# Performance work log

Hardware: AMD Instinct MI355X
Metric: run time of the kernel (lower is better)

## Reference

```python
import jax, jax.numpy as jnp
import numpy as np

# Dimensions (match init_kwargs / input_specs)
B, T, D, H, HH, E, L = 256, 512, 256, 256, 128, 32, 2


def setup_inputs() -> dict:
    key = jax.random.key(0)
    ks = jax.random.split(key, 8)
    f32 = jnp.float32
    s_ih = 1.0 / np.sqrt(D)
    s_hh = 1.0 / np.sqrt(H)
    s_hy = 1.0 / np.sqrt(D + H)
    s_hh_hy = 1.0 / np.sqrt(HH)
    s_z = 1.0 / np.sqrt(HH)
    s_d = 1.0 / np.sqrt(E)
    return {
        "input": jax.random.normal(ks[0], (B, T, D), f32),
        # main-cell weights, stacked over layers (layer1 input = hidden = D)
        "Wih": jax.random.normal(ks[1], (L, H, D), f32) * s_ih,
        "Whh": jax.random.normal(ks[2], (L, H, H), f32) * s_hh,
        "b": jnp.zeros((L, H), f32),
        # hyper (meta) RNN cell: input is concat(x_t, h_{t-1})
        "Wih_hy": jax.random.normal(ks[3], (L, HH, D + H), f32) * s_hy,
        "Whh_hy": jax.random.normal(ks[4], (L, HH, HH), f32) * s_hh_hy,
        "b_hy": jnp.zeros((L, HH), f32),
        # embedding projections: hyper_h -> z for (x-scale, h-scale, bias), then z -> d
        "Whz": jax.random.normal(ks[5], (L, 3, E, HH), f32) * s_z,
        "bz": jnp.ones((L, 3, E), f32),  # init z to 1 so d starts near a plain RNN
        "Wzd": jax.random.normal(ks[6], (L, 3, H, E), f32) * s_d,
    }


def reference(input, Wih, Whh, b, Wih_hy, Whh_hy, b_hy, Whz, bz, Wzd):
    """MetaRNN (HyperNetwork-conditioned RNN): for each layer, a small hyper RNN
    consumes [x_t, h_{t-1}] and emits embeddings z that generate per-unit scales
    d_x, d_h and a dynamic bias d_b for the main tanh RNN cell.
    Returns (all hidden states [B,T,H], last hidden state [B,H])."""
    Bb = input.shape[0]
    dt = input.dtype
    x_seq = input
    for l in range(L):
        # input-to-hidden GEMM for the whole sequence, hoisted out of the scan
        xW = jnp.einsum('btd,hd->bth', x_seq, Wih[l])  # [B,T,H]
        Whh_l, b_l = Whh[l], b[l]
        Wih_hy_l, Whh_hy_l, b_hy_l = Wih_hy[l], Whh_hy[l], b_hy[l]
        Whz_l, bz_l, Wzd_l = Whz[l], bz[l], Wzd[l]

        def step(carry, inp):
            h, hh = carry           # main hidden [B,H], hyper hidden [B,HH]
            x_t, xW_t = inp
            hyp_in = jnp.concatenate([x_t, h], axis=1)          # [B, D+H]
            hh_new = jnp.tanh(hyp_in @ Wih_hy_l.T + hh @ Whh_hy_l.T + b_hy_l)
            z = jnp.einsum('bk,gek->bge', hh_new, Whz_l) + bz_l  # [B,3,E]
            d = jnp.einsum('bge,ghe->bgh', z, Wzd_l)             # [B,3,H]
            h_new = jnp.tanh(d[:, 0] * xW_t + d[:, 1] * (h @ Whh_l.T)
                             + d[:, 2] + b_l)
            return (h_new, hh_new), h_new

        h0 = jnp.zeros((Bb, H), dt)
        hh0 = jnp.zeros((Bb, HH), dt)
        xs = (jnp.swapaxes(x_seq, 0, 1), jnp.swapaxes(xW, 0, 1))  # time-major
        _, ys = jax.lax.scan(step, (h0, hh0), xs)
        x_seq = jnp.swapaxes(ys, 0, 1)  # [B,T,H]
    return (x_seq, x_seq[:, -1, :])
```

## Files before the change

kernel.cpp:

```cpp
#include <hip/hip_runtime.h>


#define DEVI __device__ __forceinline__

typedef __bf16 bf16x8 __attribute__((ext_vector_type(8)));
typedef float f32x4 __attribute__((ext_vector_type(4)));
typedef unsigned short u16;
typedef unsigned int u32;
typedef u32 u32x4 __attribute__((ext_vector_type(4)));
typedef u16 u16x8 __attribute__((ext_vector_type(8)));

constexpr int B_ = 256, T_ = 512, D_ = 256, H_ = 256, HH_ = 128, E_ = 32;
constexpr int BT = B_ * T_;

constexpr int OXW = 0,      PXW = 16 * 8 * 512;
constexpr int OXH = 131072, PXH = 8 * 8 * 512;
constexpr int OHY = 196608, PHY = 8 * 12 * 512;
constexpr int OWHH = 294912, PWHH = 16 * 8 * 512;
constexpr int OWHZ = 425984, PWHZ = 6 * 4 * 512;
constexpr int OWZD = 450560, PWZD = 48 * 512;
constexpr int LSTRIDE = 499712;

constexpr size_t WS_XW = 0;
constexpr size_t WS_XH = (size_t)BT * H_ * 4;
constexpr size_t WS_FR = WS_XH + (size_t)BT * HH_ * 4;

DEVI u16 f2bf(float v) {
  u32 u = __float_as_uint(v);
  u += 0x7fffu + ((u >> 16) & 1u);
  return (u16)(u >> 16);
}
DEVI float bf2f(u16 s) { return __uint_as_float(((u32)s) << 16); }
DEVI void split2(float v, u16 &hi, u16 &lo) {
  hi = f2bf(v);
  lo = f2bf(v - bf2f(hi));
}
DEVI bf16x8 ldfrag(const u16 *p) {
  u32x4 v = *reinterpret_cast<const u32x4 *>(p);
  return __builtin_bit_cast(bf16x8, v);
}
DEVI void pin(bf16x8 &x) {
  u32x4 t = __builtin_bit_cast(u32x4, x);
  asm volatile("" : "+v"(t));
  x = __builtin_bit_cast(bf16x8, t);
}
DEVI f32x4 mfma3(bf16x8 ah, bf16x8 al, bf16x8 bh, bf16x8 bl, f32x4 c) {
  c = __builtin_amdgcn_mfma_f32_16x16x32_bf16(ah, bh, c, 0, 0, 0);
  c = __builtin_amdgcn_mfma_f32_16x16x32_bf16(ah, bl, c, 0, 0, 0);
  c = __builtin_amdgcn_mfma_f32_16x16x32_bf16(al, bh, c, 0, 0, 0);
  return c;
}
DEVI float tanh_fast(float x) {
  float e = __expf(2.0f * x);
  return 1.0f - 2.0f / (e + 1.0f);
}
DEVI void block_sync() {
  asm volatile("s_waitcnt lgkmcnt(0)\n\ts_barrier" ::: "memory");
}

__global__ void metarnn_prep(const float *__restrict__ Wih,
                             const float *__restrict__ Whh,
                             const float *__restrict__ Wih_hy,
                             const float *__restrict__ Whh_hy,
                             const float *__restrict__ Whz,
                             const float *__restrict__ Wzd,
                             u16 *__restrict__ fr) {
  int gid = blockIdx.x * 256 + threadIdx.x;
  int lane = gid & 63;
  int e = gid >> 6;
  if (e >= 2 * 488) return;
  int l = e / 488, r = e - l * 488;
  u16 *base = fr + (size_t)l * LSTRIDE;
  int rowL = lane & 15, kg = (lane >> 4) << 3;

  const float *src = nullptr;
  int ld = 0, nt = 0, kt = 0, KT = 1, special = 0;
  u16 *dh = nullptr, *dl = nullptr;
  if (r < 128) {
    nt = r >> 3; kt = r & 7; KT = 8;
    src = Wih + (size_t)l * H_ * D_; ld = D_;
    dh = base + OXW; dl = dh + PXW;
  } else if (r < 192) {
    r -= 128; nt = r >> 3; kt = r & 7; KT = 8;
    src = Wih_hy + (size_t)l * HH_ * (D_ + H_); ld = D_ + H_;
    dh = base + OXH; dl = dh + PXH;
  } else if (r < 288) {
    r -= 192; nt = r / 12; kt = r - nt * 12; KT = 12; special = 1;
    dh = base + OHY; dl = dh + PHY;
  } else if (r < 416) {
    r -= 288; nt = r >> 3; kt = r & 7; KT = 8;
    src = Whh + (size_t)l * H_ * H_; ld = H_;
    dh = base + OWHH; dl = dh + PWHH;
  } else if (r < 440) {
    r -= 416; nt = r >> 2; kt = r & 3; KT = 4;
    src = Whz + (size_t)l * 3 * E_ * HH_; ld = HH_;
    dh = base + OWHZ; dl = dh + PWHZ;
  } else {
    r -= 440; int g = r >> 4; nt = r & 15; kt = 0; KT = 1;
    src = Wzd + (size_t)(l * 3 + g) * H_ * E_; ld = E_;
    dh = base + OWZD + g * 16 * 512; dl = base + OWZD + PWZD + g * 16 * 512;
  }
  int row = nt * 16 + rowL;
  long dof = ((long)(nt * KT + kt) * 64 + lane) * 8;
  for (int j = 0; j < 8; ++j) {
    int k = kt * 32 + kg + j;
    float v;
    if (special) {
      v = (k < 256) ? Wih_hy[((size_t)l * HH_ + row) * (D_ + H_) + 256 + k]
                    : Whh_hy[((size_t)l * HH_ + row) * HH_ + (k - 256)];
    } else {
      v = src[(size_t)row * ld + k];
    }
    u16 hi, lo;
    split2(v, hi, lo);
    dh[dof + j] = hi;
    dl[dof + j] = lo;
  }
}

__global__ __launch_bounds__(256, 1) void metarnn_gemm(
    const float *__restrict__ x, const u16 *__restrict__ fr,
    float *__restrict__ xW, float *__restrict__ xH) {
  int w = threadIdx.x >> 6, lane = threadIdx.x & 63;
  int m0 = blockIdx.x * 32;
  int rowL = lane & 15, kg = (lane >> 4) << 3;
  f32x4 acc[2][6] = {};
  const u16 *fxw_h = fr + OXW, *fxw_l = fxw_h + PXW;
  const u16 *fxh_h = fr + OXH, *fxh_l = fxh_h + PXH;

  for (int kt = 0; kt < 8; ++kt) {
    bf16x8 ah[2], al[2];
    for (int s = 0; s < 2; ++s) {
      const float *xp = x + (size_t)(m0 + s * 16 + rowL) * 256 + kt * 32 + kg;
      u16x8 vh, vl;
#pragma unroll
      for (int j = 0; j < 8; ++j) {
        u16 hi, lo;
        split2(xp[j], hi, lo);
        vh[j] = hi; vl[j] = lo;
      }
      ah[s] = __builtin_bit_cast(bf16x8, vh);
      al[s] = __builtin_bit_cast(bf16x8, vl);
    }
#pragma unroll
    for (int q = 0; q < 6; ++q) {
      int nt = w * 6 + q;
      long o = (nt < 16) ? ((long)(nt * 8 + kt) * 64 + lane) * 8
                         : ((long)((nt - 16) * 8 + kt) * 64 + lane) * 8;
      const u16 *bh = (nt < 16) ? fxw_h + o : fxh_h + o;
      const u16 *bl = (nt < 16) ? fxw_l + o : fxh_l + o;
      bf16x8 B0 = ldfrag(bh), B1 = ldfrag(bl);
      acc[0][q] = mfma3(ah[0], al[0], B0, B1, acc[0][q]);
      acc[1][q] = mfma3(ah[1], al[1], B0, B1, acc[1][q]);
    }
  }
  for (int s = 0; s < 2; ++s)
    for (int q = 0; q < 6; ++q) {
      int nt = w * 6 + q;
#pragma unroll
      for (int r = 0; r < 4; ++r) {
        int row = m0 + s * 16 + (lane >> 4) * 4 + r;
        if (nt < 16)
          xW[(size_t)row * H_ + nt * 16 + rowL] = acc[s][q][r];
        else
          xH[(size_t)row * HH_ + (nt - 16) * 16 + rowL] = acc[s][q][r];
      }
    }
}

__global__ __launch_bounds__(512, 2) void metarnn_scan(
    const float *__restrict__ xW, const float *__restrict__ xH,
    const u16 *__restrict__ fr, const float *__restrict__ bmain,
    const float *__restrict__ bhy, const float *__restrict__ bz,
    float *__restrict__ y, float *__restrict__ hlast, int layer, int isLast) {
  __shared__ __align__(16) u16 hc_h[8 * 512];
  __shared__ __align__(16) u16 hc_l[8 * 512];
  __shared__ __align__(16) u16 hhb_h[2][4 * 512];
  __shared__ __align__(16) u16 hhb_l[2][4 * 512];
  __shared__ __align__(16) u16 zf_h[3 * 512];
  __shared__ __align__(16) u16 zf_l[3 * 512];
  __shared__ __align__(16) u16 hy_lds[8 * 12 * 512];

  int tid = threadIdx.x, w = tid >> 6, lane = tid & 63;
  int bs = blockIdx.x * 16;
  int rowL = lane & 15, colG = lane >> 4;

  const u16 *FHY = fr + OHY, *FHYl = FHY + PHY;
  const u16 *FWH = fr + OWHH, *FWHl = FWH + PWHH;
  const u16 *FWZ = fr + OWHZ, *FWZl = FWZ + PWHZ;
  const u16 *FZD = fr + OWZD, *FZDl = FZD + PWZD;

  for (int i = tid; i < 8 * 512; i += 512) { hc_h[i] = 0; hc_l[i] = 0; }
  for (int i = tid; i < 4 * 512; i += 512) {
    hhb_h[0][i] = 0; hhb_l[0][i] = 0; hhb_h[1][i] = 0; hhb_l[1][i] = 0;
  }
  for (int i = tid; i < 3 * 512; i += 512) { zf_h[i] = 0; zf_l[i] = 0; }
  for (int i = tid; i < 8 * 12 * 512 / 8; i += 512) {
    *reinterpret_cast<u32x4 *>(&hy_lds[(size_t)i * 8]) =
        *reinterpret_cast<const u32x4 *>(FHY + (size_t)i * 8);
  }

  bf16x8 RWH[2][8], RWL[2][8];
#pragma unroll
  for (int p = 0; p < 2; ++p)
#pragma unroll
    for (int kt = 0; kt < 8; ++kt) {
      long o = ((long)((2 * w + p) * 8 + kt) * 64 + lane) * 8;
      RWH[p][kt] = ldfrag(FWH + o);  pin(RWH[p][kt]);
      RWL[p][kt] = ldfrag(FWHl + o); pin(RWL[p][kt]);
    }
  bf16x8 zresH[4], zresL[4];
  {
    int wz = (w < 6) ? w : 0;
#pragma unroll
    for (int kk = 0; kk < 4; ++kk) {
      long o = ((long)(wz * 4 + kk) * 64 + lane) * 8;
      zresH[kk] = ldfrag(FWZ + o);  pin(zresH[kk]);
      zresL[kk] = ldfrag(FWZl + o); pin(zresL[kk]);
    }
  }

  int c2 = 16 * w + rowL;
  float bhv = bhy[layer * HH_ + c2];
  float bzv = (w < 6) ? bz[layer * 3 * E_ + c2] : 0.0f;
  float bbv[2];
  bbv[0] = bmain[layer * H_ + 32 * w + rowL];
  bbv[1] = bmain[layer * H_ + 32 * w + 16 + rowL];

  bf16x8 bYL[4];
#define LOAD_Y(PTR, S, KT)                                                    \
  bYL[S] = ldfrag((PTR) + ((long)(w * 12 + (KT)) * 64 + lane) * 8);
#pragma unroll
  for (int s = 0; s < 4; ++s) { LOAD_Y(FHYl, s, s) }

  float xhv[4], xwv[2][4];
#pragma unroll
  for (int r = 0; r < 4; ++r) {
    size_t row = (size_t)(bs + 4 * colG + r) * T_;
    xhv[r] = xH[row * HH_ + c2];
    xwv[0][r] = xW[row * H_ + 32 * w + rowL];
    xwv[1][r] = xW[row * H_ + 32 * w + 16 + rowL];
  }

  __syncthreads();

  for (int t = 0; t < T_; ++t) {
    const int pr = t & 1;
    const u16 *fhyl = FHYl, *fzd = FZD, *fzdl = FZDl;
    asm volatile("" : "+s"(fhyl), "+s"(fzd), "+s"(fzdl));

    f32x4 aAe = {}, aAo = {}, aW0 = {}, aW1 = {};
    __builtin_amdgcn_s_setprio(1);
#pragma unroll
    for (int j = 0; j < 12; ++j) {
      const int s4 = j & 3;
      bf16x8 ah, al;
      if (j < 8) {
        ah = ldfrag(&hc_h[j * 512 + lane * 8]);
        al = ldfrag(&hc_l[j * 512 + lane * 8]);
      } else {
        ah = ldfrag(&hhb_h[pr ^ 1][(j - 8) * 512 + lane * 8]);
        al = ldfrag(&hhb_l[pr ^ 1][(j - 8) * 512 + lane * 8]);
      }
      bf16x8 yh = ldfrag(&hy_lds[(w * 12 + j) * 512 + lane * 8]);
      if (j & 1) aAo = mfma3(ah, al, yh, bYL[s4], aAo);
      else       aAe = mfma3(ah, al, yh, bYL[s4], aAe);
      if (j < 8) {
        aW0 = mfma3(ah, al, RWH[0][j], RWL[0][j], aW0);
        aW1 = mfma3(ah, al, RWH[1][j], RWL[1][j], aW1);
        LOAD_Y(fhyl, s4, j + 4)
      } else {
        LOAD_Y(fhyl, s4, j - 8)
      }
    }
    __builtin_amdgcn_s_setprio(0);
    f32x4 aA;
#pragma unroll
    for (int r = 0; r < 4; ++r) aA[r] = aAe[r] + aAo[r];

    bf16x8 D0h[2], D0l[2];
#pragma unroll
    for (int p = 0; p < 2; ++p) {
      long o = ((long)(2 * w + p) * 64 + lane) * 8;
      D0h[p] = ldfrag(fzd + o);
      D0l[p] = ldfrag(fzdl + o);
    }

    {
      int kfr = w >> 1;
      int hb2 = 2 * (w & 1) + (rowL >> 3);
      int j7 = rowL & 7;
#pragma unroll
      for (int r = 0; r < 4; ++r) {
        float v = tanh_fast(aA[r] + xhv[r] + bhv);
        u16 hi, lo;
        split2(v, hi, lo);
        int di = kfr * 512 + ((4 * colG + r) + 16 * hb2) * 8 + j7;
        hhb_h[pr][di] = hi;
        hhb_l[pr][di] = lo;
      }
    }
#pragma unroll
    for (int r = 0; r < 4; ++r) {
      xhv[r] = xH[((size_t)(bs + 4 * colG + r) * T_ + t + 1) * HH_ + c2];
    }
    block_sync();

    bf16x8 D1h[2], D1l[2], D2h[2], D2l[2];
#pragma unroll
    for (int p = 0; p < 2; ++p) {
      long o1 = ((long)(16 + 2 * w + p) * 64 + lane) * 8;
      long o2 = ((long)(32 + 2 * w + p) * 64 + lane) * 8;
      D1h[p] = ldfrag(fzd + o1);
      D1l[p] = ldfrag(fzdl + o1);
      D2h[p] = ldfrag(fzd + o2);
      D2l[p] = ldfrag(fzdl + o2);
    }

    if (w < 6) {
      f32x4 aZ = {};
#pragma unroll
      for (int kk = 0; kk < 4; ++kk) {
        bf16x8 ah = ldfrag(&hhb_h[pr][kk * 512 + lane * 8]);
        bf16x8 al = ldfrag(&hhb_l[pr][kk * 512 + lane * 8]);
        aZ = mfma3(ah, al, zresH[kk], zresL[kk], aZ);
      }
      int g = c2 >> 5;
      int hb3 = 2 * (w & 1) + (rowL >> 3);
      int j7 = rowL & 7;
#pragma unroll
      for (int r = 0; r < 4; ++r) {
        float v = aZ[r] + bzv;
        u16 hi, lo;
        split2(v, hi, lo);
        int di = g * 512 + ((4 * colG + r) + 16 * hb3) * 8 + j7;
        zf_h[di] = hi;
        zf_l[di] = lo;
      }
    }
    block_sync();

    float arg[2][4];
#pragma unroll
    for (int p = 0; p < 2; ++p)
#pragma unroll
      for (int r = 0; r < 4; ++r) arg[p][r] = bbv[p];
    {
      bf16x8 zh = ldfrag(&zf_h[0 * 512 + lane * 8]);
      bf16x8 zl = ldfrag(&zf_l[0 * 512 + lane * 8]);
#pragma unroll
      for (int p = 0; p < 2; ++p) {
        f32x4 zero = {};
        f32x4 dg = mfma3(zh, zl, D0h[p], D0l[p], zero);
#pragma unroll
        for (int r = 0; r < 4; ++r) arg[p][r] += dg[r] * xwv[p][r];
      }
    }
#pragma unroll
    for (int r = 0; r < 4; ++r) {
      size_t row = (size_t)(bs + 4 * colG + r) * T_ + t + 1;
      xwv[0][r] = xW[row * H_ + 32 * w + rowL];
      xwv[1][r] = xW[row * H_ + 32 * w + 16 + rowL];
    }
    {
      bf16x8 zh = ldfrag(&zf_h[1 * 512 + lane * 8]);
      bf16x8 zl = ldfrag(&zf_l[1 * 512 + lane * 8]);
#pragma unroll
      for (int p = 0; p < 2; ++p) {
        f32x4 zero = {};
        f32x4 dg = mfma3(zh, zl, D1h[p], D1l[p], zero);
#pragma unroll
        for (int r = 0; r < 4; ++r)
          arg[p][r] += dg[r] * ((p == 0) ? aW0[r] : aW1[r]);
      }
    }
    {
      bf16x8 zh = ldfrag(&zf_h[2 * 512 + lane * 8]);
      bf16x8 zl = ldfrag(&zf_l[2 * 512 + lane * 8]);
#pragma unroll
      for (int p = 0; p < 2; ++p) {
        f32x4 zero = {};
        f32x4 dg = mfma3(zh, zl, D2h[p], D2l[p], zero);
#pragma unroll
        for (int r = 0; r < 4; ++r) arg[p][r] += dg[r];
      }
    }

#pragma unroll
    for (int p = 0; p < 2; ++p) {
      int c = 32 * w + 16 * p + rowL;
      int hb6 = 2 * p + (rowL >> 3);
      int j7 = rowL & 7;
#pragma unroll
      for (int r = 0; r < 4; ++r) {
        int m = 4 * colG + r;
        float h = tanh_fast(arg[p][r]);
        size_t gi = (size_t)(bs + m) * T_ + t;
        y[gi * H_ + c] = h;
        if (isLast && t == T_ - 1) hlast[(size_t)(bs + m) * H_ + c] = h;
        u16 hi, lo;
        split2(h, hi, lo);
        int di = (c >> 5) * 512 + (m + 16 * hb6) * 8 + j7;
        hc_h[di] = hi;
        hc_l[di] = lo;
      }
    }
    block_sync();
  }
#undef LOAD_Y
}

extern "C" void kernel_launch(void *const *d_in, const int *in_sizes, int n_in,
                              void *d_out, int out_size, void *d_ws,
                              size_t ws_size, hipStream_t stream) {
  (void)in_sizes; (void)n_in; (void)out_size; (void)ws_size;
  const float *input  = (const float *)d_in[0];
  const float *Wih    = (const float *)d_in[1];
  const float *Whh    = (const float *)d_in[2];
  const float *b      = (const float *)d_in[3];
  const float *Wih_hy = (const float *)d_in[4];
  const float *Whh_hy = (const float *)d_in[5];
  const float *b_hy   = (const float *)d_in[6];
  const float *Whz    = (const float *)d_in[7];
  const float *bz     = (const float *)d_in[8];
  const float *Wzd    = (const float *)d_in[9];

  float *out = (float *)d_out;
  float *xW = (float *)((char *)d_ws + WS_XW);
  float *xH = (float *)((char *)d_ws + WS_XH);
  u16 *fr = (u16 *)((char *)d_ws + WS_FR);
  float *hlast = out + (size_t)BT * H_;

  metarnn_prep<<<dim3(244), dim3(256), 0, stream>>>(Wih, Whh, Wih_hy, Whh_hy,
                                                    Whz, Wzd, fr);
  for (int l = 0; l < 2; ++l) {
    const float *xsrc = (l == 0) ? input : out;
    const u16 *frl = fr + (size_t)l * LSTRIDE;
    metarnn_gemm<<<dim3(BT / 32), dim3(256), 0, stream>>>(xsrc, frl, xW, xH);
    metarnn_scan<<<dim3(16), dim3(512), 0, stream>>>(
        xW, xH, frl, b, b_hy, bz, out, hlast, l, (l == 1) ? 1 : 0);
  }
}
```

Baseline: 9.273 ms.

## Split scan block into hyper and main warp groups with streamed weights

The scan kernel now runs 16 waves per block instead of 8. Waves 0-7 compute the hyper-RNN recurrence and waves 8-15 compute the main h@Whh product, so the two serial GEMM chains run concurrently. Weights are no longer staged in LDS or pinned in registers. Each wave instead streams its fragments from global memory through a small rotating register buffer, which lowers register pressure but adds global/L2 load latency inside the per-timestep loop.

```diff
diff --git a/kernel.cpp b/kernel.cpp
--- a/kernel.cpp
+++ b/kernel.cpp
@@ -38,11 +38,6 @@
 DEVI bf16x8 ldfrag(const u16 *p) {
   u32x4 v = *reinterpret_cast<const u32x4 *>(p);
   return __builtin_bit_cast(bf16x8, v);
-}
-DEVI void pin(bf16x8 &x) {
-  u32x4 t = __builtin_bit_cast(u32x4, x);
-  asm volatile("" : "+v"(t));
-  x = __builtin_bit_cast(bf16x8, t);
 }
 DEVI f32x4 mfma3(bf16x8 ah, bf16x8 al, bf16x8 bh, bf16x8 bl, f32x4 c) {
   c = __builtin_amdgcn_mfma_f32_16x16x32_bf16(ah, bh, c, 0, 0, 0);
@@ -168,162 +163,150 @@
     }
 }
 
-__global__ __launch_bounds__(512, 2) void metarnn_scan(
+__global__ __launch_bounds__(1024, 4) void metarnn_scan(
     const float *__restrict__ xW, const float *__restrict__ xH,
     const u16 *__restrict__ fr, const float *__restrict__ bmain,
     const float *__restrict__ bhy, const float *__restrict__ bz,
     float *__restrict__ y, float *__restrict__ hlast, int layer, int isLast) {
-  __shared__ __align__(16) u16 hc_h[8 * 512];
-  __shared__ __align__(16) u16 hc_l[8 * 512];
-  __shared__ __align__(16) u16 hhb_h[2][4 * 512];
-  __shared__ __align__(16) u16 hhb_l[2][4 * 512];
-  __shared__ __align__(16) u16 zf_h[3 * 512];
-  __shared__ __align__(16) u16 zf_l[3 * 512];
-  __shared__ __align__(16) u16 hy_lds[8 * 12 * 512];
+  __shared__ __align__(16) u16 hc_h[8 * 512], hc_l[8 * 512];
+  __shared__ __align__(16) u16 hhb_h[2][4 * 512], hhb_l[2][4 * 512];
+  __shared__ __align__(16) u16 zf_h[3 * 512], zf_l[3 * 512];
 
   int tid = threadIdx.x, w = tid >> 6, lane = tid & 63;
   int bs = blockIdx.x * 16;
   int rowL = lane & 15, colG = lane >> 4;
+  const bool hyper = (w < 8);
+  const int mi = w & 7;
 
   const u16 *FHY = fr + OHY, *FHYl = FHY + PHY;
   const u16 *FWH = fr + OWHH, *FWHl = FWH + PWHH;
   const u16 *FWZ = fr + OWHZ, *FWZl = FWZ + PWHZ;
   const u16 *FZD = fr + OWZD, *FZDl = FZD + PWZD;
 
-  for (int i = tid; i < 8 * 512; i += 512) { hc_h[i] = 0; hc_l[i] = 0; }
-  for (int i = tid; i < 4 * 512; i += 512) {
+  for (int i = tid; i < 8 * 512; i += 1024) { hc_h[i] = 0; hc_l[i] = 0; }
+  for (int i = tid; i < 4 * 512; i += 1024) {
     hhb_h[0][i] = 0; hhb_l[0][i] = 0; hhb_h[1][i] = 0; hhb_l[1][i] = 0;
   }
-  for (int i = tid; i < 3 * 512; i += 512) { zf_h[i] = 0; zf_l[i] = 0; }
-  for (int i = tid; i < 8 * 12 * 512 / 8; i += 512) {
-    *reinterpret_cast<u32x4 *>(&hy_lds[(size_t)i * 8]) =
-        *reinterpret_cast<const u32x4 *>(FHY + (size_t)i * 8);
-  }
-
-  bf16x8 RWH[2][8], RWL[2][8];
-#pragma unroll
-  for (int p = 0; p < 2; ++p)
-#pragma unroll
-    for (int kt = 0; kt < 8; ++kt) {
-      long o = ((long)((2 * w + p) * 8 + kt) * 64 + lane) * 8;
-      RWH[p][kt] = ldfrag(FWH + o);  pin(RWH[p][kt]);
-      RWL[p][kt] = ldfrag(FWHl + o); pin(RWL[p][kt]);
-    }
-  bf16x8 zresH[4], zresL[4];
-  {
-    int wz = (w < 6) ? w : 0;
-#pragma unroll
-    for (int kk = 0; kk < 4; ++kk) {
-      long o = ((long)(wz * 4 + kk) * 64 + lane) * 8;
-      zresH[kk] = ldfrag(FWZ + o);  pin(zresH[kk]);
-      zresL[kk] = ldfrag(FWZl + o); pin(zresL[kk]);
-    }
-  }
-
-  int c2 = 16 * w + rowL;
-  float bhv = bhy[layer * HH_ + c2];
+  for (int i = tid; i < 3 * 512; i += 1024) { zf_h[i] = 0; zf_l[i] = 0; }
+
+  int c2 = 16 * (w & 7) + rowL;
+  float bhv = hyper ? bhy[layer * HH_ + c2] : 0.0f;
   float bzv = (w < 6) ? bz[layer * 3 * E_ + c2] : 0.0f;
-  float bbv[2];
-  bbv[0] = bmain[layer * H_ + 32 * w + rowL];
-  bbv[1] = bmain[layer * H_ + 32 * w + 16 + rowL];
-
-  bf16x8 bYL[4];
-#define LOAD_Y(PTR, S, KT)                                                    \
-  bYL[S] = ldfrag((PTR) + ((long)(w * 12 + (KT)) * 64 + lane) * 8);
-#pragma unroll
-  for (int s = 0; s < 4; ++s) { LOAD_Y(FHYl, s, s) }
-
-  float xhv[4], xwv[2][4];
-#pragma unroll
-  for (int r = 0; r < 4; ++r) {
-    size_t row = (size_t)(bs + 4 * colG + r) * T_;
-    xhv[r] = xH[row * HH_ + c2];
-    xwv[0][r] = xW[row * H_ + 32 * w + rowL];
-    xwv[1][r] = xW[row * H_ + 32 * w + 16 + rowL];
+  float bbv0 = 0.0f, bbv1 = 0.0f;
+  if (!hyper) {
+    bbv0 = bmain[layer * H_ + 32 * mi + rowL];
+    bbv1 = bmain[layer * H_ + 32 * mi + 16 + rowL];
+  }
+
+  bf16x8 S[12];
+  bf16x8 Z[8];
+  if (hyper) {
+#pragma unroll
+    for (int s = 0; s < 3; ++s) {
+      long o = ((long)(w * 12 + s) * 64 + lane) * 8;
+      S[s] = ldfrag(FHY + o);
+      S[3 + s] = ldfrag(FHYl + o);
+    }
+  } else {
+#pragma unroll
+    for (int s = 0; s < 3; ++s)
+#pragma unroll
+      for (int p = 0; p < 2; ++p) {
+        long o = ((long)((2 * mi + p) * 8 + s) * 64 + lane) * 8;
+        S[4 * s + p] = ldfrag(FWH + o);
+        S[4 * s + 2 + p] = ldfrag(FWHl + o);
+      }
+  }
+
+  float xv[8];
+  if (hyper) {
+#pragma unroll
+    for (int r = 0; r < 4; ++r)
+      xv[r] = xH[((size_t)(bs + 4 * colG + r) * T_) * HH_ + c2];
+  } else {
+#pragma unroll
+    for (int r = 0; r < 4; ++r) {
+      size_t row = (size_t)(bs + 4 * colG + r) * T_;
+      xv[r] = xW[row * H_ + 32 * mi + rowL];
+      xv[4 + r] = xW[row * H_ + 32 * mi + 16 + rowL];
+    }
   }
 
   __syncthreads();
 
   for (int t = 0; t < T_; ++t) {
     const int pr = t & 1;
-    const u16 *fhyl = FHYl, *fzd = FZD, *fzdl = FZDl;
-    asm volatile("" : "+s"(fhyl), "+s"(fzd), "+s"(fzdl));
-
-    f32x4 aAe = {}, aAo = {}, aW0 = {}, aW1 = {};
-    __builtin_amdgcn_s_setprio(1);
-#pragma unroll
-    for (int j = 0; j < 12; ++j) {
-      const int s4 = j & 3;
-      bf16x8 ah, al;
-      if (j < 8) {
-        ah = ldfrag(&hc_h[j * 512 + lane * 8]);
-        al = ldfrag(&hc_l[j * 512 + lane * 8]);
-      } else {
-        ah = ldfrag(&hhb_h[pr ^ 1][(j - 8) * 512 + lane * 8]);
-        al = ldfrag(&hhb_l[pr ^ 1][(j - 8) * 512 + lane * 8]);
-      }
-      bf16x8 yh = ldfrag(&hy_lds[(w * 12 + j) * 512 + lane * 8]);
-      if (j & 1) aAo = mfma3(ah, al, yh, bYL[s4], aAo);
-      else       aAe = mfma3(ah, al, yh, bYL[s4], aAe);
-      if (j < 8) {
-        aW0 = mfma3(ah, al, RWH[0][j], RWL[0][j], aW0);
-        aW1 = mfma3(ah, al, RWH[1][j], RWL[1][j], aW1);
-        LOAD_Y(fhyl, s4, j + 4)
-      } else {
-        LOAD_Y(fhyl, s4, j - 8)
-      }
-    }
-    __builtin_amdgcn_s_setprio(0);
-    f32x4 aA;
-#pragma unroll
-    for (int r = 0; r < 4; ++r) aA[r] = aAe[r] + aAo[r];
-
-    bf16x8 D0h[2], D0l[2];
-#pragma unroll
-    for (int p = 0; p < 2; ++p) {
-      long o = ((long)(2 * w + p) * 64 + lane) * 8;
-      D0h[p] = ldfrag(fzd + o);
-      D0l[p] = ldfrag(fzdl + o);
-    }
-
-    {
-      int kfr = w >> 1;
-      int hb2 = 2 * (w & 1) + (rowL >> 3);
-      int j7 = rowL & 7;
-#pragma unroll
-      for (int r = 0; r < 4; ++r) {
-        float v = tanh_fast(aA[r] + xhv[r] + bhv);
-        u16 hi, lo;
-        split2(v, hi, lo);
-        int di = kfr * 512 + ((4 * colG + r) + 16 * hb2) * 8 + j7;
-        hhb_h[pr][di] = hi;
-        hhb_l[pr][di] = lo;
-      }
-    }
-#pragma unroll
-    for (int r = 0; r < 4; ++r) {
-      xhv[r] = xH[((size_t)(bs + 4 * colG + r) * T_ + t + 1) * HH_ + c2];
+    f32x4 acc0 = {}, acc1 = {};
+
+    if (hyper) {
+      __builtin_amdgcn_s_setprio(1);
+#pragma unroll
+      for (int j = 0; j < 12; ++j) {
+        const int s = j % 3;
+        bf16x8 ah, al;
+        if (j < 8) {
+          ah = ldfrag(&hc_h[j * 512 + lane * 8]);
+          al = ldfrag(&hc_l[j * 512 + lane * 8]);
+        } else {
+          ah = ldfrag(&hhb_h[pr ^ 1][(j - 8) * 512 + lane * 8]);
+          al = ldfrag(&hhb_l[pr ^ 1][(j - 8) * 512 + lane * 8]);
+        }
+        if (j & 1) acc1 = mfma3(ah, al, S[s], S[3 + s], acc1);
+        else       acc0 = mfma3(ah, al, S[s], S[3 + s], acc0);
+        const int ktp = (j < 9) ? j + 3 : j - 9;
+        long o = ((long)(w * 12 + ktp) * 64 + lane) * 8;
+        S[s] = ldfrag(FHY + o);
+        S[3 + s] = ldfrag(FHYl + o);
+      }
+      __builtin_amdgcn_s_setprio(0);
+      {
+        int kfr = w >> 1;
+        int hb2 = 2 * (w & 1) + (rowL >> 3);
+        int j7 = rowL & 7;
+#pragma unroll
+        for (int r = 0; r < 4; ++r) {
+          float v = tanh_fast((acc0[r] + acc1[r]) + xv[r] + bhv);
+          u16 hi, lo;
+          split2(v, hi, lo);
+          int di = kfr * 512 + ((4 * colG + r) + 16 * hb2) * 8 + j7;
+          hhb_h[pr][di] = hi;
+          hhb_l[pr][di] = lo;
+        }
+      }
+    } else {
+      __builtin_amdgcn_s_setprio(1);
+#pragma unroll
+      for (int j = 0; j < 8; ++j) {
+        const int s = j % 3;
+        bf16x8 ah = ldfrag(&hc_h[j * 512 + lane * 8]);
+        bf16x8 al = ldfrag(&hc_l[j * 512 + lane * 8]);
+        acc0 = mfma3(ah, al, S[4 * s + 0], S[4 * s + 2], acc0);
+        acc1 = mfma3(ah, al, S[4 * s + 1], S[4 * s + 3], acc1);
+        const int ktp = (j < 5) ? j + 3 : ((j == 5) ? 2 : ((j == 6) ? 0 : 1));
+#pragma unroll
+        for (int p = 0; p < 2; ++p) {
+          long o = ((long)((2 * mi + p) * 8 + ktp) * 64 + lane) * 8;
+          S[4 * s + p] = ldfrag(FWH + o);
+          S[4 * s + 2 + p] = ldfrag(FWHl + o);
+        }
+      }
+      __builtin_amdgcn_s_setprio(0);
     }
     block_sync();
 
-    bf16x8 D1h[2], D1l[2], D2h[2], D2l[2];
-#pragma unroll
-    for (int p = 0; p < 2; ++p) {
-      long o1 = ((long)(16 + 2 * w + p) * 64 + lane) * 8;
-      long o2 = ((long)(32 + 2 * w + p) * 64 + lane) * 8;
-      D1h[p] = ldfrag(fzd + o1);
-      D1l[p] = ldfrag(fzdl + o1);
-      D2h[p] = ldfrag(fzd + o2);
-      D2l[p] = ldfrag(fzdl + o2);
-    }
-
     if (w < 6) {
+#pragma unroll
+      for (int kk = 0; kk < 4; ++kk) {
+        long o = ((long)(w * 4 + kk) * 64 + lane) * 8;
+        Z[kk] = ldfrag(FWZ + o);
+        Z[4 + kk] = ldfrag(FWZl + o);
+      }
       f32x4 aZ = {};
 #pragma unroll
       for (int kk = 0; kk < 4; ++kk) {
         bf16x8 ah = ldfrag(&hhb_h[pr][kk * 512 + lane * 8]);
         bf16x8 al = ldfrag(&hhb_l[pr][kk * 512 + lane * 8]);
-        aZ = mfma3(ah, al, zresH[kk], zresL[kk], aZ);
+        aZ = mfma3(ah, al, Z[kk], Z[4 + kk], aZ);
       }
       int g = c2 >> 5;
       int hb3 = 2 * (w & 1) + (rowL >> 3);
@@ -338,76 +321,108 @@
         zf_l[di] = lo;
       }
     }
+    if (!hyper) {
+#pragma unroll
+      for (int p = 0; p < 2; ++p) {
+        long o = ((long)(2 * mi + p) * 64 + lane) * 8;
+        Z[p] = ldfrag(FZD + o);
+        Z[2 + p] = ldfrag(FZDl + o);
+      }
+    }
     block_sync();
 
-    float arg[2][4];
-#pragma unroll
-    for (int p = 0; p < 2; ++p)
-#pragma unroll
-      for (int r = 0; r < 4; ++r) arg[p][r] = bbv[p];
-    {
-      bf16x8 zh = ldfrag(&zf_h[0 * 512 + lane * 8]);
-      bf16x8 zl = ldfrag(&zf_l[0 * 512 + lane * 8]);
+    if (hyper) {
+      const int tn = (t + 1 < T_) ? t + 1 : t;
+#pragma unroll
+      for (int r = 0; r < 4; ++r)
+        xv[r] = xH[((size_t)(bs + 4 * colG + r) * T_ + tn) * HH_ + c2];
+    } else {
+      float arg[2][4];
+#pragma unroll
+      for (int r = 0; r < 4; ++r) { arg[0][r] = bbv0; arg[1][r] = bbv1; }
+      {
+        bf16x8 zh = ldfrag(&zf_h[lane * 8]);
+        bf16x8 zl = ldfrag(&zf_l[lane * 8]);
+        f32x4 dg0[2];
+#pragma unroll
+        for (int p = 0; p < 2; ++p) {
+          f32x4 zero = {};
+          dg0[p] = mfma3(zh, zl, Z[p], Z[2 + p], zero);
+        }
+#pragma unroll
+        for (int p = 0; p < 2; ++p) {
+          long o = ((long)(16 + 2 * mi + p) * 64 + lane) * 8;
+          Z[4 + p] = ldfrag(FZD + o);
+          Z[6 + p] = ldfrag(FZDl + o);
+        }
+#pragma unroll
+        for (int p = 0; p < 2; ++p)
+#pragma unroll
+          for (int r = 0; r < 4; ++r) arg[p][r] += dg0[p][r] * xv[p * 4 + r];
+      }
+      {
+        bf16x8 zh = ldfrag(&zf_h[512 + lane * 8]);
+        bf16x8 zl = ldfrag(&zf_l[512 + lane * 8]);
+        f32x4 dg1[2];
+#pragma unroll
+        for (int p = 0; p < 2; ++p) {
+          f32x4 zero = {};
+          dg1[p] = mfma3(zh, zl, Z[4 + p], Z[6 + p], zero);
+        }
+#pragma unroll
+        for (int p = 0; p < 2; ++p) {
+          long o = ((long)(32 + 2 * mi + p) * 64 + lane) * 8;
+          Z[p] = ldfrag(FZD + o);
+          Z[2 + p] = ldfrag(FZDl + o);
+        }
+#pragma unroll
+        for (int r = 0; r < 4; ++r) {
+          arg[0][r] += dg1[0][r] * acc0[r];
+          arg[1][r] += dg1[1][r] * acc1[r];
+        }
+      }
+      {
+        bf16x8 zh = ldfrag(&zf_h[2 * 512 + lane * 8]);
+        bf16x8 zl = ldfrag(&zf_l[2 * 512 + lane * 8]);
+#pragma unroll
+        for (int p = 0; p < 2; ++p) {
+          f32x4 zero = {};
+          f32x4 dg = mfma3(zh, zl, Z[p], Z[2 + p], zero);
+#pragma unroll
+          for (int r = 0; r < 4; ++r) arg[p][r] += dg[r];
+        }
+      }
+      {
+        const int tn = (t + 1 < T_) ? t + 1 : t;
+#pragma unroll
+        for (int r = 0; r < 4; ++r) {
+          size_t row = (size_t)(bs + 4 * colG + r) * T_ + tn;
+          xv[r] = xW[row * H_ + 32 * mi + rowL];
+          xv[4 + r] = xW[row * H_ + 32 * mi + 16 + rowL];
+        }
+      }
 #pragma unroll
       for (int p = 0; p < 2; ++p) {
-        f32x4 zero = {};
-        f32x4 dg = mfma3(zh, zl, D0h[p], D0l[p], zero);
-#pragma unroll
-        for (int r = 0; r < 4; ++r) arg[p][r] += dg[r] * xwv[p][r];
-      }
-    }
-#pragma unroll
-    for (int r = 0; r < 4; ++r) {
-      size_t row = (size_t)(bs + 4 * colG + r) * T_ + t + 1;
-      xwv[0][r] = xW[row * H_ + 32 * w + rowL];
-      xwv[1][r] = xW[row * H_ + 32 * w + 16 + rowL];
-    }
-    {
-      bf16x8 zh = ldfrag(&zf_h[1 * 512 + lane * 8]);
-      bf16x8 zl = ldfrag(&zf_l[1 * 512 + lane * 8]);
-#pragma unroll
-      for (int p = 0; p < 2; ++p) {
-        f32x4 zero = {};
-        f32x4 dg = mfma3(zh, zl, D1h[p], D1l[p], zero);
-#pragma unroll
-        for (int r = 0; r < 4; ++r)
-          arg[p][r] += dg[r] * ((p == 0) ? aW0[r] : aW1[r]);
-      }
-    }
-    {
-      bf16x8 zh = ldfrag(&zf_h[2 * 512 + lane * 8]);
-      bf16x8 zl = ldfrag(&zf_l[2 * 512 + lane * 8]);
-#pragma unroll
-      for (int p = 0; p < 2; ++p) {
-        f32x4 zero = {};
-        f32x4 dg = mfma3(zh, zl, D2h[p], D2l[p], zero);
-#pragma unroll
-        for (int r = 0; r < 4; ++r) arg[p][r] += dg[r];
-      }
-    }
-
-#pragma unroll
-    for (int p = 0; p < 2; ++p) {
-      int c = 32 * w + 16 * p + rowL;
-      int hb6 = 2 * p + (rowL >> 3);
-      int j7 = rowL & 7;
-#pragma unroll
-      for (int r = 0; r < 4; ++r) {
-        int m = 4 * colG + r;
-        float h = tanh_fast(arg[p][r]);
-        size_t gi = (size_t)(bs + m) * T_ + t;
-        y[gi * H_ + c] = h;
-        if (isLast && t == T_ - 1) hlast[(size_t)(bs + m) * H_ + c] = h;
-        u16 hi, lo;
-        split2(h, hi, lo);
-        int di = (c >> 5) * 512 + (m + 16 * hb6) * 8 + j7;
-        hc_h[di] = hi;
-        hc_l[di] = lo;
+        int c = 32 * mi + 16 * p + rowL;
+        int hb6 = 2 * p + (rowL >> 3);
+        int j7 = rowL & 7;
+#pragma unroll
+        for (int r = 0; r < 4; ++r) {
+          int m = 4 * colG + r;
+          float h = tanh_fast(arg[p][r]);
+          size_t gi = (size_t)(bs + m) * T_ + t;
+          y[gi * H_ + c] = h;
+          if (isLast && t == T_ - 1) hlast[(size_t)(bs + m) * H_ + c] = h;
+          u16 hi, lo;
+          split2(h, hi, lo);
+          int di = (c >> 5) * 512 + (m + 16 * hb6) * 8 + j7;
+          hc_h[di] = hi;
+          hc_l[di] = lo;
+        }
       }
     }
     block_sync();
   }
-#undef LOAD_Y
 }
 
 extern "C" void kernel_launch(void *const *d_in, const int *in_sizes, int n_in,
@@ -437,7 +452,7 @@
     const float *xsrc = (l == 0) ? input : out;
     const u16 *frl = fr + (size_t)l * LSTRIDE;
     metarnn_gemm<<<dim3(BT / 32), dim3(256), 0, stream>>>(xsrc, frl, xW, xH);
-    metarnn_scan<<<dim3(16), dim3(512), 0, stream>>>(
+    metarnn_scan<<<dim3(16), dim3(1024), 0, stream>>>(
         xW, xH, frl, b, b_hy, bz, out, hlast, l, (l == 1) ? 1 : 0);
   }
 }
```

Measured after the change: 17.39 ms. +87.5%, slower.

## Stream Whh-hi and Whz fragments from global instead of pinning in registers

Applied to the files above, without the earlier changes.

Stops keeping the high half of the recurrent weight fragments and the z-projection fragments resident in registers. Instead it streams them from global/L2 through a rotating 3-slot buffer inside the main loop, and deepens the hyper-weight prefetch ring from 4 to 6 slots. Per-timestep xH/xW loads are now double-buffered and issued earlier, and the loads that guarded out-of-range t+1 reads are clamped. This relieves register pressure on the serial recurrence, at the cost of extra per-step global traffic and load latency on the critical path.

```diff
diff --git a/kernel.cpp b/kernel.cpp
--- a/kernel.cpp
+++ b/kernel.cpp
@@ -200,60 +200,58 @@
         *reinterpret_cast<const u32x4 *>(FHY + (size_t)i * 8);
   }
 
-  bf16x8 RWH[2][8], RWL[2][8];
+  bf16x8 RWL[2][8];
 #pragma unroll
   for (int p = 0; p < 2; ++p)
 #pragma unroll
     for (int kt = 0; kt < 8; ++kt) {
       long o = ((long)((2 * w + p) * 8 + kt) * 64 + lane) * 8;
-      RWH[p][kt] = ldfrag(FWH + o);  pin(RWH[p][kt]);
-      RWL[p][kt] = ldfrag(FWHl + o); pin(RWL[p][kt]);
-    }
-  bf16x8 zresH[4], zresL[4];
-  {
-    int wz = (w < 6) ? w : 0;
-#pragma unroll
-    for (int kk = 0; kk < 4; ++kk) {
-      long o = ((long)(wz * 4 + kk) * 64 + lane) * 8;
-      zresH[kk] = ldfrag(FWZ + o);  pin(zresH[kk]);
-      zresL[kk] = ldfrag(FWZl + o); pin(zresL[kk]);
-    }
-  }
+      RWL[p][kt] = ldfrag(FWHl + o);
+      pin(RWL[p][kt]);
+    }
 
   int c2 = 16 * w + rowL;
+  int wz = (w < 6) ? w : 0;
   float bhv = bhy[layer * HH_ + c2];
   float bzv = (w < 6) ? bz[layer * 3 * E_ + c2] : 0.0f;
   float bbv[2];
   bbv[0] = bmain[layer * H_ + 32 * w + rowL];
   bbv[1] = bmain[layer * H_ + 32 * w + 16 + rowL];
 
-  bf16x8 bYL[4];
-#define LOAD_Y(PTR, S, KT)                                                    \
-  bYL[S] = ldfrag((PTR) + ((long)(w * 12 + (KT)) * 64 + lane) * 8);
-#pragma unroll
-  for (int s = 0; s < 4; ++s) { LOAD_Y(FHYl, s, s) }
-
-  float xhv[4], xwv[2][4];
+  bf16x8 bWH[3][2];
+  bf16x8 bYL[6];
+#define LOAD_W(S, KT)                                                         \
+  {                                                                           \
+    long o0 = ((long)((2 * w) * 8 + (KT)) * 64 + lane) * 8;                   \
+    long o1 = ((long)((2 * w + 1) * 8 + (KT)) * 64 + lane) * 8;               \
+    bWH[S][0] = ldfrag(FWH + o0);                                             \
+    bWH[S][1] = ldfrag(FWH + o1);                                             \
+  }
+#define LOAD_Y(S, KT)                                                         \
+  bYL[S] = ldfrag(FHYl + ((long)(w * 12 + (KT)) * 64 + lane) * 8);
+#pragma unroll
+  for (int s = 0; s < 3; ++s) LOAD_W(s, s)
+#pragma unroll
+  for (int s = 0; s < 6; ++s) { LOAD_Y(s, s) }
+
+  float xhA[4], xwA[2][4], xhB[4], xwB[2][4];
 #pragma unroll
   for (int r = 0; r < 4; ++r) {
     size_t row = (size_t)(bs + 4 * colG + r) * T_;
-    xhv[r] = xH[row * HH_ + c2];
-    xwv[0][r] = xW[row * H_ + 32 * w + rowL];
-    xwv[1][r] = xW[row * H_ + 32 * w + 16 + rowL];
+    xhA[r] = xH[row * HH_ + c2];
+    xwA[0][r] = xW[row * H_ + 32 * w + rowL];
+    xwA[1][r] = xW[row * H_ + 32 * w + 16 + rowL];
   }
 
   __syncthreads();
 
   for (int t = 0; t < T_; ++t) {
     const int pr = t & 1;
-    const u16 *fhyl = FHYl, *fzd = FZD, *fzdl = FZDl;
-    asm volatile("" : "+s"(fhyl), "+s"(fzd), "+s"(fzdl));
-
     f32x4 aAe = {}, aAo = {}, aW0 = {}, aW1 = {};
     __builtin_amdgcn_s_setprio(1);
 #pragma unroll
     for (int j = 0; j < 12; ++j) {
-      const int s4 = j & 3;
+      const int s3 = j % 3, s6 = j % 6;
       bf16x8 ah, al;
       if (j < 8) {
         ah = ldfrag(&hc_h[j * 512 + lane * 8]);
@@ -263,27 +261,35 @@
         al = ldfrag(&hhb_l[pr ^ 1][(j - 8) * 512 + lane * 8]);
       }
       bf16x8 yh = ldfrag(&hy_lds[(w * 12 + j) * 512 + lane * 8]);
-      if (j & 1) aAo = mfma3(ah, al, yh, bYL[s4], aAo);
-      else       aAe = mfma3(ah, al, yh, bYL[s4], aAe);
+      if (j & 1) aAo = mfma3(ah, al, yh, bYL[s6], aAo);
+      else       aAe = mfma3(ah, al, yh, bYL[s6], aAe);
       if (j < 8) {
-        aW0 = mfma3(ah, al, RWH[0][j], RWL[0][j], aW0);
-        aW1 = mfma3(ah, al, RWH[1][j], RWL[1][j], aW1);
-        LOAD_Y(fhyl, s4, j + 4)
-      } else {
-        LOAD_Y(fhyl, s4, j - 8)
-      }
+        aW0 = mfma3(ah, al, bWH[s3][0], RWL[0][j], aW0);
+        aW1 = mfma3(ah, al, bWH[s3][1], RWL[1][j], aW1);
+      }
+      if (j < 6) { LOAD_Y(s6, j + 6) } else { LOAD_Y(s6, j - 6) }
+      if (j < 5) LOAD_W(s3, j + 3)
     }
     __builtin_amdgcn_s_setprio(0);
     f32x4 aA;
 #pragma unroll
     for (int r = 0; r < 4; ++r) aA[r] = aAe[r] + aAo[r];
 
+#pragma unroll
+    for (int s = 0; s < 3; ++s) LOAD_W(s, s)
+    bf16x8 zS[4], zSl[4];
+#pragma unroll
+    for (int kk = 0; kk < 4; ++kk) {
+      long o = ((long)(wz * 4 + kk) * 64 + lane) * 8;
+      zS[kk] = ldfrag(FWZ + o);
+      zSl[kk] = ldfrag(FWZl + o);
+    }
     bf16x8 D0h[2], D0l[2];
 #pragma unroll
     for (int p = 0; p < 2; ++p) {
       long o = ((long)(2 * w + p) * 64 + lane) * 8;
-      D0h[p] = ldfrag(fzd + o);
-      D0l[p] = ldfrag(fzdl + o);
+      D0h[p] = ldfrag(FZD + o);
+      D0l[p] = ldfrag(FZDl + o);
     }
 
     {
@@ -292,7 +298,7 @@
       int j7 = rowL & 7;
 #pragma unroll
       for (int r = 0; r < 4; ++r) {
-        float v = tanh_fast(aA[r] + xhv[r] + bhv);
+        float v = tanh_fast(aA[r] + xhA[r] + bhv);
         u16 hi, lo;
         split2(v, hi, lo);
         int di = kfr * 512 + ((4 * colG + r) + 16 * hb2) * 8 + j7;
@@ -300,10 +306,6 @@
         hhb_l[pr][di] = lo;
       }
     }
-#pragma unroll
-    for (int r = 0; r < 4; ++r) {
-      xhv[r] = xH[((size_t)(bs + 4 * colG + r) * T_ + t + 1) * HH_ + c2];
-    }
     block_sync();
 
     bf16x8 D1h[2], D1l[2], D2h[2], D2l[2];
@@ -311,10 +313,20 @@
     for (int p = 0; p < 2; ++p) {
       long o1 = ((long)(16 + 2 * w + p) * 64 + lane) * 8;
       long o2 = ((long)(32 + 2 * w + p) * 64 + lane) * 8;
-      D1h[p] = ldfrag(fzd + o1);
-      D1l[p] = ldfrag(fzdl + o1);
-      D2h[p] = ldfrag(fzd + o2);
-      D2l[p] = ldfrag(fzdl + o2);
+      D1h[p] = ldfrag(FZD + o1);
+      D1l[p] = ldfrag(FZDl + o1);
+      D2h[p] = ldfrag(FZD + o2);
+      D2l[p] = ldfrag(FZDl + o2);
+    }
+    {
+      const int tn = (t + 1 < T_) ? t + 1 : t;
+#pragma unroll
+      for (int r = 0; r < 4; ++r) {
+        size_t row = (size_t)(bs + 4 * colG + r) * T_ + tn;
+        xhB[r] = xH[row * HH_ + c2];
+        xwB[0][r] = xW[row * H_ + 32 * w + rowL];
+        xwB[1][r] = xW[row * H_ + 32 * w + 16 + rowL];
+      }
     }
 
     if (w < 6) {
@@ -323,7 +335,7 @@
       for (int kk = 0; kk < 4; ++kk) {
         bf16x8 ah = ldfrag(&hhb_h[pr][kk * 512 + lane * 8]);
         bf16x8 al = ldfrag(&hhb_l[pr][kk * 512 + lane * 8]);
-        aZ = mfma3(ah, al, zresH[kk], zresL[kk], aZ);
+        aZ = mfma3(ah, al, zS[kk], zSl[kk], aZ);
       }
       int g = c2 >> 5;
       int hb3 = 2 * (w & 1) + (rowL >> 3);
@@ -353,14 +365,8 @@
         f32x4 zero = {};
         f32x4 dg = mfma3(zh, zl, D0h[p], D0l[p], zero);
 #pragma unroll
-        for (int r = 0; r < 4; ++r) arg[p][r] += dg[r] * xwv[p][r];
-      }
-    }
-#pragma unroll
-    for (int r = 0; r < 4; ++r) {
-      size_t row = (size_t)(bs + 4 * colG + r) * T_ + t + 1;
-      xwv[0][r] = xW[row * H_ + 32 * w + rowL];
-      xwv[1][r] = xW[row * H_ + 32 * w + 16 + rowL];
+        for (int r = 0; r < 4; ++r) arg[p][r] += dg[r] * xwA[p][r];
+      }
     }
     {
       bf16x8 zh = ldfrag(&zf_h[1 * 512 + lane * 8]);
@@ -406,7 +412,15 @@
       }
     }
     block_sync();
-  }
+
+#pragma unroll
+    for (int r = 0; r < 4; ++r) {
+      xhA[r] = xhB[r];
+      xwA[0][r] = xwB[0][r];
+      xwA[1][r] = xwB[1][r];
+    }
+  }
+#undef LOAD_W
 #undef LOAD_Y
 }
 
```

Measured after the change: 10.35 ms. 1.12x slower.
